# Performance work log

Hardware: AMD Instinct MI355X
Metric: run time of the kernel (lower is better)

## Reference

```python
import jax, jax.numpy as jnp
import numpy as np
from jax import lax

KS = 21        # kernel_size
FS = 32        # sampling frequency: grid = linspace(0, KS/FS, KS)
FEATURES = 3   # = input channels (depthwise Gaussian)
CHUNK = 2304   # lax.map batch_size over flattened pixels (6912 = 3 chunks)
L = 1.0        # self.l


def gaussian_kernels(gamma):
    """Per-feature isotropic Gaussian taps, energy-normalized. -> (KS,KS,1,F) HWIO depthwise."""
    x = jnp.linspace(0.0, KS / FS, KS)
    xx, yy = jnp.meshgrid(x, x)
    mean = KS / (2.0 * FS)
    sigma = 1.0 / gamma                      # (F,)
    r2 = (xx - mean) ** 2 + (yy - mean) ** 2  # (KS,KS)
    amp = (FS ** 2) / (2.0 * jnp.pi * sigma ** 2)
    k = amp * jnp.exp(-r2[..., None] / (2.0 * sigma ** 2))   # (KS,KS,F)
    # normalize_energy=True: unit L2 energy per feature
    k = k / jnp.sqrt((k ** 2).sum(axis=(0, 1), keepdims=True))
    return k[:, :, None, :]


def gauss_conv(x, gamma):
    """Depthwise Gaussian blur, NHWC, SAME padding, stride 1."""
    k = gaussian_kernels(gamma).astype(x.dtype)
    return lax.conv_general_dilated(
        x, k, window_strides=(1, 1), padding='SAME',
        dimension_numbers=('NHWC', 'HWIO', 'NHWC'),
        feature_group_count=x.shape[-1])


def setup_inputs() -> dict:
    key = jax.random.key(0)
    k1, k2, k3, k4 = jax.random.split(key, 4)
    inputs = jax.random.uniform(k1, (4, 48, 48, 3), dtype=jnp.float32)
    gamma_m = jax.random.uniform(k2, (FEATURES,), jnp.float32, 0.2, 2.0)
    gamma_w = jax.random.uniform(k3, (FEATURES,), jnp.float32, 0.2, 2.0)
    gamma_g = jax.random.uniform(k4, (FEATURES,), jnp.float32, 0.2, 2.0)
    return {"inputs": inputs, "gamma_m": gamma_m, "gamma_w": gamma_w, "gamma_g": gamma_g}


def _per_image_diffs(img, blur):
    """For each scalar pixel x of img: mean over ALL of blur of tanh(x - blur)."""
    bf = blur.reshape(-1)                     # (Nb,)
    flat = img.reshape(-1)                    # (N,)
    chunks = flat.reshape(-1, CHUNK)          # (N/CHUNK, CHUNK)

    def f(ch):  # (CHUNK,) -> (CHUNK,)  ; tile is (CHUNK, Nb)
        return jnp.tanh(ch[:, None] - bf[None, :]).mean(axis=-1)

    return lax.map(f, chunks).reshape(img.shape)


def _inrf(inputs, gamma_m, gamma_w, gamma_g):
    first_term = gauss_conv(inputs, gamma_m)          # M(inputs)
    blurred = gauss_conv(inputs, gamma_g)             # G(inputs)
    # sequential over batch (mirrors lax.scan over leading axis)
    difference = lax.map(lambda t: _per_image_diffs(t[0], t[1]), (inputs, blurred))
    second_term = gauss_conv(difference, gamma_w)     # W(difference)
    return first_term - L * second_term


def reference(inputs, gamma_m, gamma_w, gamma_g):
    return _inrf(inputs, gamma_m, gamma_w, gamma_g)
```

## Files before the change

kernel.cpp:

```cpp
#include <hip/hip_runtime.h>

#define KS   21
#define HH   48
#define WW   48
#define CC   3
#define ROW  (WW*CC)
#define NB   4
#define NPIX (HH*WW*CC)
#define NTOT (NB*NPIX)
#define TPB  256
#define NBLK (NTOT/TPB)
#define SEGS (NPIX/TPB)
#define CTAN 2.8853900817779268f
#define B_HI 5.0f
#define B_LO -4.0f

__device__ __forceinline__ float fast_exp2(float x) {
#if __has_builtin(__builtin_amdgcn_exp2f)
    return __builtin_amdgcn_exp2f(x);
#else
    return __expf(x * 0.6931471805599453f);
#endif
}
__device__ __forceinline__ float fast_rcp(float x) {
#if __has_builtin(__builtin_amdgcn_rcpf)
    return __builtin_amdgcn_rcpf(x);
#else
    return 1.0f / x;
#endif
}

__device__ __forceinline__ float tap1d(const float* g, int f, int i) {
    float sigma  = 1.0f / g[f];
    float inv2s2 = 0.5f / (sigma * sigma);
    const float step = 21.0f / 640.0f, mean = 21.0f / 64.0f;
    float r = (float)i * step - mean;
    float v = expf(-r * r * inv2s2);
    float ss = 0.0f;
    for (int j = 0; j < KS; ++j) {
        float rj = (float)j * step - mean;
        float vj = expf(-rj * rj * inv2s2);
        ss += vj * vj;
    }
    return v * rsqrtf(ss);
}

__global__ __launch_bounds__(TPB) void hconv_mg(
    const float* __restrict__ in, const float* __restrict__ gm,
    const float* __restrict__ gg, float* __restrict__ hm, float* __restrict__ hg)
{
    __shared__ float sm[63], sg[63];
    const int t = threadIdx.x;
    if (t < 126) {
        int set = t / 63, f = (t % 63) / 21, i = t % 21;
        float v = tap1d(set ? gg : gm, f, i);
        (set ? sg : sm)[t % 63] = v;
    }
    __syncthreads();
    const int idx = blockIdx.x * TPB + t;
    const int c = idx % CC, w = (idx / CC) % WW;
    const int rowstart = idx - w * CC;
    float tm[KS], tg[KS];
#pragma unroll
    for (int k = 0; k < KS; ++k) { tm[k] = sm[c * 21 + k]; tg[k] = sg[c * 21 + k]; }
    float am = 0.f, ag = 0.f;
#pragma unroll
    for (int k = 0; k < KS; ++k) {
        int wc = w + k - 10;
        int wcc = min(max(wc, 0), WW - 1);
        float v = in[rowstart + wcc * CC];
        bool ok = (unsigned)wc < (unsigned)WW;
        am = fmaf(v, ok ? tm[k] : 0.f, am);
        ag = fmaf(v, ok ? tg[k] : 0.f, ag);
    }
    hm[idx] = am;
    hg[idx] = ag;
}

__global__ __launch_bounds__(TPB) void vconv_mg(
    const float* __restrict__ hm, const float* __restrict__ hg,
    const float* __restrict__ gm, const float* __restrict__ gg,
    float* __restrict__ first, float* __restrict__ active,
    int* __restrict__ segcnt, int* __restrict__ netcnt,
    float* __restrict__ diffsum)
{
    __shared__ float sm[63], sg[63];
    __shared__ int wcnt[4], wnet[4];
    const int t = threadIdx.x;
    if (t < 126) {
        int set = t / 63, f = (t % 63) / 21, i = t % 21;
        float v = tap1d(set ? gg : gm, f, i);
        (set ? sg : sm)[t % 63] = v;
    }
    __syncthreads();
    const int idx = blockIdx.x * TPB + t;
    const int c = idx % CC, h = (idx / ROW) % HH;
    const int n = blockIdx.x / SEGS, seg = blockIdx.x % SEGS;
    float tm[KS], tg[KS];
#pragma unroll
    for (int k = 0; k < KS; ++k) { tm[k] = sm[c * 21 + k]; tg[k] = sg[c * 21 + k]; }
    float am = 0.f, ag = 0.f;
#pragma unroll
    for (int k = 0; k < KS; ++k) {
        int hc = h + k - 10;
        int hcc = min(max(hc, 0), HH - 1);
        int off = idx + (hcc - h) * ROW;
        bool ok = (unsigned)hc < (unsigned)HH;
        am = fmaf(hm[off], ok ? tm[k] : 0.f, am);
        ag = fmaf(hg[off], ok ? tg[k] : 0.f, ag);
    }
    first[idx] = am;
    diffsum[idx] = 0.0f;

    const float b = ag;
    const bool satpos = (b <= B_LO);
    const bool satneg = (b >= B_HI);
    const bool act = !(satpos || satneg);
    const int lane = t & 63, wid = t >> 6;
    unsigned long long mb = __ballot(act);
    int cnt = __popcll(mb);
    int netc = __popcll(__ballot(satpos)) - __popcll(__ballot(satneg));
    if (lane == 0) { wcnt[wid] = cnt; wnet[wid] = netc; }
    __syncthreads();
    int pre = 0;
    for (int j = 0; j < wid; ++j) pre += wcnt[j];
    if (act) {
        int pos = pre + __popcll(mb & ((1ull << lane) - 1ull));
        active[n * NPIX + seg * TPB + pos] = CTAN * b;
    }
    if (t == 0) {
        segcnt[blockIdx.x] = wcnt[0] + wcnt[1] + wcnt[2] + wcnt[3];
        netcnt[blockIdx.x] = wnet[0] + wnet[1] + wnet[2] + wnet[3];
    }
}

__global__ __launch_bounds__(TPB) void diff_kernel(
    const float* __restrict__ in, const float* __restrict__ active,
    const int* __restrict__ segcnt, float* __restrict__ diffsum)
{
    const int n = blockIdx.y, seg = blockIdx.z;
    const int len = segcnt[n * SEGS + seg];
    if (len == 0) return;
    __shared__ float sb[TPB];
    const int t = threadIdx.x;
    if (t < len) sb[t] = active[n * NPIX + seg * TPB + t];
    __syncthreads();
    const int p = blockIdx.x * TPB + t;
    float cx = CTAN * in[n * NPIX + p];
    float acc = 0.0f;
#pragma unroll 4
    for (int q = 0; q < len; ++q)
        acc += fast_rcp(fast_exp2(cx - sb[q]) + 1.0f);
    atomicAdd(&diffsum[n * NPIX + p], (float)len - 2.0f * acc);
}

__global__ __launch_bounds__(TPB) void hconv_w(
    const float* __restrict__ diffsum, const float* __restrict__ gw,
    const int* __restrict__ netcnt, float* __restrict__ tmp)
{
    __shared__ float sw[63];
    const int t = threadIdx.x;
    if (t < 63) sw[t] = tap1d(gw, t / 21, t % 21);
    __syncthreads();
    const int idx = blockIdx.x * TPB + t;
    const int c = idx % CC, w = (idx / CC) % WW;
    const int n = blockIdx.x / SEGS;
    float netf = 0.f;
    for (int s = 0; s < SEGS; ++s) netf += (float)netcnt[n * SEGS + s];
    const int rowstart = idx - w * CC;
    float tw[KS];
#pragma unroll
    for (int k = 0; k < KS; ++k) tw[k] = sw[c * 21 + k];
    float a = 0.f;
#pragma unroll
    for (int k = 0; k < KS; ++k) {
        int wc = w + k - 10;
        int wcc = min(max(wc, 0), WW - 1);
        float v = diffsum[rowstart + wcc * CC] + netf;
        bool ok = (unsigned)wc < (unsigned)WW;
        a = fmaf(v, ok ? tw[k] : 0.f, a);
    }
    tmp[idx] = a * (1.0f / (float)NPIX);
}

__global__ __launch_bounds__(TPB) void vconv_w_sub(
    const float* __restrict__ tmp, const float* __restrict__ gw,
    const float* __restrict__ first, float* __restrict__ out)
{
    __shared__ float sw[63];
    const int t = threadIdx.x;
    if (t < 63) sw[t] = tap1d(gw, t / 21, t % 21);
    __syncthreads();
    const int idx = blockIdx.x * TPB + t;
    const int c = idx % CC, h = (idx / ROW) % HH;
    float tw[KS];
#pragma unroll
    for (int k = 0; k < KS; ++k) tw[k] = sw[c * 21 + k];
    float a = 0.f;
#pragma unroll
    for (int k = 0; k < KS; ++k) {
        int hc = h + k - 10;
        int hcc = min(max(hc, 0), HH - 1);
        bool ok = (unsigned)hc < (unsigned)HH;
        a = fmaf(tmp[idx + (hcc - h) * ROW], ok ? tw[k] : 0.f, a);
    }
    out[idx] = first[idx] - a;
}

extern "C" void kernel_launch(void* const* d_in, const int* in_sizes, int n_in,
                              void* d_out, int out_size, void* d_ws, size_t ws_size,
                              hipStream_t stream) {
    const float* in = (const float*)d_in[0];
    const float* gm = (const float*)d_in[1];
    const float* gw = (const float*)d_in[2];
    const float* gg = (const float*)d_in[3];
    float* out = (float*)d_out;

    float* wsf     = (float*)d_ws;
    float* hm      = wsf;
    float* hg      = hm + NTOT;
    float* first   = hg + NTOT;
    float* active  = first + NTOT;
    float* diffsum = active + NTOT;
    float* tmp     = diffsum + NTOT;
    int*   segcnt  = (int*)(tmp + NTOT);
    int*   netcnt  = segcnt + NBLK;

    hconv_mg<<<NBLK, TPB, 0, stream>>>(in, gm, gg, hm, hg);
    vconv_mg<<<NBLK, TPB, 0, stream>>>(hm, hg, gm, gg, first, active, segcnt, netcnt, diffsum);
    diff_kernel<<<dim3(SEGS, NB, SEGS), TPB, 0, stream>>>(in, active, segcnt, diffsum);
    hconv_w<<<NBLK, TPB, 0, stream>>>(diffsum, gw, netcnt, tmp);
    vconv_w_sub<<<NBLK, TPB, 0, stream>>>(tmp, gw, first, out);
}
```

Baseline: 79.32 us.

## Fuse entire INRF pipeline into one per-image kernel using shared memory

Replaces the five-kernel pipeline with a single kernel that gives each image one 576-thread block. Every block stages its image in padded LDS planes and runs the separable blurs with register sliding windows of 12 outputs per thread. The active-pixel compaction and the pairwise tanh sum are also done in LDS. This removes the global intermediates, the launch overheads and the atomics. The cost is that only four blocks cover the whole device, so the quadratic pairwise term runs on four CUs instead of thousands of blocks.

```diff
diff --git a/kernel.cpp b/kernel.cpp
--- a/kernel.cpp
+++ b/kernel.cpp
@@ -4,13 +4,14 @@
 #define HH   48
 #define WW   48
 #define CC   3
-#define ROW  (WW*CC)
 #define NB   4
 #define NPIX (HH*WW*CC)
 #define NTOT (NB*NPIX)
-#define TPB  256
-#define NBLK (NTOT/TPB)
-#define SEGS (NPIX/TPB)
+#define TPB  576
+#define PXT  12
+#define SPAN (PXT + KS - 1)
+#define PST  49
+#define PLANE (HH*PST)
 #define CTAN 2.8853900817779268f
 #define B_HI 5.0f
 #define B_LO -4.0f
@@ -45,166 +46,146 @@
     return v * rsqrtf(ss);
 }
 
-__global__ __launch_bounds__(TPB) void hconv_mg(
+__device__ __forceinline__ void hconv(const float* src, float* dst,
+                                      const float* taps, int t) {
+    const int c = t / 192, rem = t % 192, h = rem >> 2, w0 = (rem & 3) * PXT;
+    const float* row = src + c * PLANE + h * PST;
+    float v[SPAN];
+#pragma unroll
+    for (int s = 0; s < SPAN; ++s) {
+        int w = w0 - 10 + s;
+        v[s] = ((unsigned)w < (unsigned)WW) ? row[w] : 0.0f;
+    }
+    float tp[KS];
+#pragma unroll
+    for (int k = 0; k < KS; ++k) tp[k] = taps[c * 21 + k];
+    float* drow = dst + c * PLANE + h * PST + w0;
+#pragma unroll
+    for (int j = 0; j < PXT; ++j) {
+        float a = 0.0f;
+#pragma unroll
+        for (int k = 0; k < KS; ++k) a = fmaf(v[j + k], tp[k], a);
+        drow[j] = a;
+    }
+}
+
+__device__ __forceinline__ void vconv(const float* src, const float* taps,
+                                      int t, float* acc) {
+    const int c = t / 192, rem = t % 192, h0 = (rem / 48) * PXT, w = rem % 48;
+    const float* col = src + c * PLANE + w;
+    float v[SPAN];
+#pragma unroll
+    for (int s = 0; s < SPAN; ++s) {
+        int h = h0 - 10 + s;
+        v[s] = ((unsigned)h < (unsigned)HH) ? col[h * PST] : 0.0f;
+    }
+    float tp[KS];
+#pragma unroll
+    for (int k = 0; k < KS; ++k) tp[k] = taps[c * 21 + k];
+#pragma unroll
+    for (int j = 0; j < PXT; ++j) {
+        float a = 0.0f;
+#pragma unroll
+        for (int k = 0; k < KS; ++k) a = fmaf(v[j + k], tp[k], a);
+        acc[j] = a;
+    }
+}
+
+__global__ __launch_bounds__(TPB) void inrf_fused(
     const float* __restrict__ in, const float* __restrict__ gm,
-    const float* __restrict__ gg, float* __restrict__ hm, float* __restrict__ hg)
+    const float* __restrict__ gw, const float* __restrict__ gg,
+    float* __restrict__ out)
 {
-    __shared__ float sm[63], sg[63];
+    __shared__ float bufI[CC * PLANE];
+    __shared__ float bufB[CC * PLANE];
+    __shared__ float sm[63], sg[63], sw[63];
+    __shared__ int s_len, s_net;
+
     const int t = threadIdx.x;
-    if (t < 126) {
+    const int n = blockIdx.x;
+    const int lane = t & 63;
+
+    if (t < 189) {
         int set = t / 63, f = (t % 63) / 21, i = t % 21;
-        float v = tap1d(set ? gg : gm, f, i);
-        (set ? sg : sm)[t % 63] = v;
-    }
-    __syncthreads();
-    const int idx = blockIdx.x * TPB + t;
-    const int c = idx % CC, w = (idx / CC) % WW;
-    const int rowstart = idx - w * CC;
-    float tm[KS], tg[KS];
-#pragma unroll
-    for (int k = 0; k < KS; ++k) { tm[k] = sm[c * 21 + k]; tg[k] = sg[c * 21 + k]; }
-    float am = 0.f, ag = 0.f;
-#pragma unroll
-    for (int k = 0; k < KS; ++k) {
-        int wc = w + k - 10;
-        int wcc = min(max(wc, 0), WW - 1);
-        float v = in[rowstart + wcc * CC];
-        bool ok = (unsigned)wc < (unsigned)WW;
-        am = fmaf(v, ok ? tm[k] : 0.f, am);
-        ag = fmaf(v, ok ? tg[k] : 0.f, ag);
-    }
-    hm[idx] = am;
-    hg[idx] = ag;
-}
-
-__global__ __launch_bounds__(TPB) void vconv_mg(
-    const float* __restrict__ hm, const float* __restrict__ hg,
-    const float* __restrict__ gm, const float* __restrict__ gg,
-    float* __restrict__ first, float* __restrict__ active,
-    int* __restrict__ segcnt, int* __restrict__ netcnt,
-    float* __restrict__ diffsum)
-{
-    __shared__ float sm[63], sg[63];
-    __shared__ int wcnt[4], wnet[4];
-    const int t = threadIdx.x;
-    if (t < 126) {
-        int set = t / 63, f = (t % 63) / 21, i = t % 21;
-        float v = tap1d(set ? gg : gm, f, i);
-        (set ? sg : sm)[t % 63] = v;
-    }
-    __syncthreads();
-    const int idx = blockIdx.x * TPB + t;
-    const int c = idx % CC, h = (idx / ROW) % HH;
-    const int n = blockIdx.x / SEGS, seg = blockIdx.x % SEGS;
-    float tm[KS], tg[KS];
-#pragma unroll
-    for (int k = 0; k < KS; ++k) { tm[k] = sm[c * 21 + k]; tg[k] = sg[c * 21 + k]; }
-    float am = 0.f, ag = 0.f;
-#pragma unroll
-    for (int k = 0; k < KS; ++k) {
-        int hc = h + k - 10;
-        int hcc = min(max(hc, 0), HH - 1);
-        int off = idx + (hcc - h) * ROW;
-        bool ok = (unsigned)hc < (unsigned)HH;
-        am = fmaf(hm[off], ok ? tm[k] : 0.f, am);
-        ag = fmaf(hg[off], ok ? tg[k] : 0.f, ag);
-    }
-    first[idx] = am;
-    diffsum[idx] = 0.0f;
-
-    const float b = ag;
-    const bool satpos = (b <= B_LO);
-    const bool satneg = (b >= B_HI);
-    const bool act = !(satpos || satneg);
-    const int lane = t & 63, wid = t >> 6;
-    unsigned long long mb = __ballot(act);
-    int cnt = __popcll(mb);
-    int netc = __popcll(__ballot(satpos)) - __popcll(__ballot(satneg));
-    if (lane == 0) { wcnt[wid] = cnt; wnet[wid] = netc; }
-    __syncthreads();
-    int pre = 0;
-    for (int j = 0; j < wid; ++j) pre += wcnt[j];
-    if (act) {
-        int pos = pre + __popcll(mb & ((1ull << lane) - 1ull));
-        active[n * NPIX + seg * TPB + pos] = CTAN * b;
-    }
-    if (t == 0) {
-        segcnt[blockIdx.x] = wcnt[0] + wcnt[1] + wcnt[2] + wcnt[3];
-        netcnt[blockIdx.x] = wnet[0] + wnet[1] + wnet[2] + wnet[3];
-    }
-}
-
-__global__ __launch_bounds__(TPB) void diff_kernel(
-    const float* __restrict__ in, const float* __restrict__ active,
-    const int* __restrict__ segcnt, float* __restrict__ diffsum)
-{
-    const int n = blockIdx.y, seg = blockIdx.z;
-    const int len = segcnt[n * SEGS + seg];
-    if (len == 0) return;
-    __shared__ float sb[TPB];
-    const int t = threadIdx.x;
-    if (t < len) sb[t] = active[n * NPIX + seg * TPB + t];
-    __syncthreads();
-    const int p = blockIdx.x * TPB + t;
-    float cx = CTAN * in[n * NPIX + p];
-    float acc = 0.0f;
-#pragma unroll 4
-    for (int q = 0; q < len; ++q)
-        acc += fast_rcp(fast_exp2(cx - sb[q]) + 1.0f);
-    atomicAdd(&diffsum[n * NPIX + p], (float)len - 2.0f * acc);
-}
-
-__global__ __launch_bounds__(TPB) void hconv_w(
-    const float* __restrict__ diffsum, const float* __restrict__ gw,
-    const int* __restrict__ netcnt, float* __restrict__ tmp)
-{
-    __shared__ float sw[63];
-    const int t = threadIdx.x;
-    if (t < 63) sw[t] = tap1d(gw, t / 21, t % 21);
-    __syncthreads();
-    const int idx = blockIdx.x * TPB + t;
-    const int c = idx % CC, w = (idx / CC) % WW;
-    const int n = blockIdx.x / SEGS;
-    float netf = 0.f;
-    for (int s = 0; s < SEGS; ++s) netf += (float)netcnt[n * SEGS + s];
-    const int rowstart = idx - w * CC;
-    float tw[KS];
-#pragma unroll
-    for (int k = 0; k < KS; ++k) tw[k] = sw[c * 21 + k];
-    float a = 0.f;
-#pragma unroll
-    for (int k = 0; k < KS; ++k) {
-        int wc = w + k - 10;
-        int wcc = min(max(wc, 0), WW - 1);
-        float v = diffsum[rowstart + wcc * CC] + netf;
-        bool ok = (unsigned)wc < (unsigned)WW;
-        a = fmaf(v, ok ? tw[k] : 0.f, a);
-    }
-    tmp[idx] = a * (1.0f / (float)NPIX);
-}
-
-__global__ __launch_bounds__(TPB) void vconv_w_sub(
-    const float* __restrict__ tmp, const float* __restrict__ gw,
-    const float* __restrict__ first, float* __restrict__ out)
-{
-    __shared__ float sw[63];
-    const int t = threadIdx.x;
-    if (t < 63) sw[t] = tap1d(gw, t / 21, t % 21);
-    __syncthreads();
-    const int idx = blockIdx.x * TPB + t;
-    const int c = idx % CC, h = (idx / ROW) % HH;
-    float tw[KS];
-#pragma unroll
-    for (int k = 0; k < KS; ++k) tw[k] = sw[c * 21 + k];
-    float a = 0.f;
-#pragma unroll
-    for (int k = 0; k < KS; ++k) {
-        int hc = h + k - 10;
-        int hcc = min(max(hc, 0), HH - 1);
-        bool ok = (unsigned)hc < (unsigned)HH;
-        a = fmaf(tmp[idx + (hcc - h) * ROW], ok ? tw[k] : 0.f, a);
-    }
-    out[idx] = first[idx] - a;
+        const float* g = (set == 0) ? gm : (set == 1) ? gg : gw;
+        float v = tap1d(g, f, i);
+        ((set == 0) ? sm : (set == 1) ? sg : sw)[t % 63] = v;
+    }
+    if (t == 0) { s_len = 0; s_net = 0; }
+
+    const float* imgp = in + n * NPIX;
+#pragma unroll
+    for (int k = 0; k < PXT; ++k) {
+        int j = k * TPB + t;
+        int c = j % 3, hw = j / 3, w = hw % WW, h = hw / WW;
+        bufI[c * PLANE + h * PST + w] = imgp[j];
+    }
+    __syncthreads();
+
+    hconv(bufI, bufB, sm, t);
+    __syncthreads();
+    float first[PXT];
+    vconv(bufB, sm, t, first);
+    __syncthreads();
+
+    hconv(bufI, bufB, sg, t);
+    __syncthreads();
+    float bb[PXT];
+    vconv(bufB, sg, t, bb);
+    __syncthreads();
+
+    int wnet = 0;
+#pragma unroll
+    for (int j = 0; j < PXT; ++j) {
+        bool sp = (bb[j] <= B_LO);
+        bool sn = (bb[j] >= B_HI);
+        unsigned long long bp = __ballot(sp), bn = __ballot(sn);
+        if (lane == 0) wnet += __popcll(bp) - __popcll(bn);
+        if (!(sp | sn)) {
+            int pos = atomicAdd(&s_len, 1);
+            bufB[pos] = CTAN * bb[j];
+        }
+    }
+    if (lane == 0) atomicAdd(&s_net, wnet);
+    __syncthreads();
+
+    const int len = s_len;
+    const float netf = (float)s_net;
+
+    {
+        const int c = t / 192, rem = t % 192, h0 = (rem / 48) * PXT, w = rem % 48;
+        float* col = bufI + c * PLANE + w;
+#pragma unroll
+        for (int j = 0; j < PXT; ++j) {
+            float cx = CTAN * col[(h0 + j) * PST];
+            float acc = 0.0f;
+            for (int q = 0; q < len; ++q)
+                acc += fast_rcp(fast_exp2(cx - bufB[q]) + 1.0f);
+            col[(h0 + j) * PST] = (netf + (float)len - 2.0f * acc) * (1.0f / (float)NPIX);
+        }
+    }
+    __syncthreads();
+
+    hconv(bufI, bufB, sw, t);
+    __syncthreads();
+    float second[PXT];
+    vconv(bufB, sw, t, second);
+    __syncthreads();
+
+    {
+        const int c = t / 192, rem = t % 192, h0 = (rem / 48) * PXT, w = rem % 48;
+#pragma unroll
+        for (int j = 0; j < PXT; ++j)
+            bufI[c * PLANE + (h0 + j) * PST + w] = first[j] - second[j];
+    }
+    __syncthreads();
+    float* outp = out + n * NPIX;
+#pragma unroll
+    for (int k = 0; k < PXT; ++k) {
+        int j = k * TPB + t;
+        int c = j % 3, hw = j / 3, w = hw % WW, h = hw / WW;
+        outp[j] = bufI[c * PLANE + h * PST + w];
+    }
 }
 
 extern "C" void kernel_launch(void* const* d_in, const int* in_sizes, int n_in,
@@ -215,20 +196,7 @@
     const float* gw = (const float*)d_in[2];
     const float* gg = (const float*)d_in[3];
     float* out = (float*)d_out;
-
-    float* wsf     = (float*)d_ws;
-    float* hm      = wsf;
-    float* hg      = hm + NTOT;
-    float* first   = hg + NTOT;
-    float* active  = first + NTOT;
-    float* diffsum = active + NTOT;
-    float* tmp     = diffsum + NTOT;
-    int*   segcnt  = (int*)(tmp + NTOT);
-    int*   netcnt  = segcnt + NBLK;
-
-    hconv_mg<<<NBLK, TPB, 0, stream>>>(in, gm, gg, hm, hg);
-    vconv_mg<<<NBLK, TPB, 0, stream>>>(hm, hg, gm, gg, first, active, segcnt, netcnt, diffsum);
-    diff_kernel<<<dim3(SEGS, NB, SEGS), TPB, 0, stream>>>(in, active, segcnt, diffsum);
-    hconv_w<<<NBLK, TPB, 0, stream>>>(diffsum, gw, netcnt, tmp);
-    vconv_w_sub<<<NBLK, TPB, 0, stream>>>(tmp, gw, first, out);
-}
+    (void)d_ws; (void)ws_size;
+
+    inrf_fused<<<NB, TPB, 0, stream>>>(in, gm, gw, gg, out);
+}
```

After: 301.8 us. 280% more time.
